# Kernel tuning notes

Hardware: AMD Instinct MI355X
Metric: run time of the kernel (lower is better)

## Reference

```python
import jax, jax.numpy as jnp
import numpy as np

B, L, D, H = 2, 256, 512, 8
DV = D // H
INF = 1e12

def _xavier(key, shape, fan_in, fan_out):
    a = float(np.sqrt(6.0 / (fan_in + fan_out)))
    return jax.random.uniform(key, shape, minval=-a, maxval=a, dtype=jnp.float32)

def setup_inputs() -> dict:
    key = jax.random.key(0)
    ks = jax.random.split(key, 9)
    inp = jax.random.normal(ks[0], (B, L, D), dtype=jnp.float32)
    relation_inp = jax.random.normal(ks[1], (B, L, L, D), dtype=jnp.float32)
    mask = jax.random.randint(ks[2], (B, L, L), 0, 2).astype(bool)
    adj_mask = jax.random.randint(ks[3], (B, H, L, L), 0, 2).astype(jnp.float32)
    W_value = _xavier(ks[4], (D, H * DV), D, H * DV)
    W_relation = _xavier(ks[5], (D, H * DV), D, H * DV)
    # weight vectors have torch shape (1,1,1,H,DV); xavier fans over last two dims
    w_src = _xavier(ks[6], (H, DV), H, DV)
    w_tgt = _xavier(ks[7], (H, DV), H, DV)
    w_rel = _xavier(ks[8], (H, DV), H, DV)
    return {"inp": inp, "relation_inp": relation_inp, "mask": mask,
            "adj_mask": adj_mask, "W_value": W_value, "W_relation": W_relation,
            "w_src": w_src, "w_tgt": w_tgt, "w_rel": w_rel}

def reference(inp, relation_inp, mask, adj_mask, W_value, W_relation, w_src, w_tgt, w_rel):
    b, l, d = inp.shape
    h, dv = w_src.shape
    # value: (B,H,L,DV)
    value = (inp @ W_value).reshape(b, l, h, dv).transpose(0, 2, 1, 3)
    # relation: (B,L,L,H,DV)
    relation = (relation_inp @ W_relation).reshape(b, l, l, h, dv)
    # scores[b,h,i,j] = w_src.v_j + w_tgt.v_i + w_rel.rel[b,i,j,h]
    s_src = jnp.einsum('bhjd,hd->bhj', value, w_src)[:, :, None, :]
    s_tgt = jnp.einsum('bhid,hd->bhi', value, w_tgt)[:, :, :, None]
    s_rel = jnp.einsum('bijhd,hd->bhij', relation, w_rel)
    scores = s_src + s_tgt + s_rel
    scores = jnp.where(scores >= 0, scores, 0.2 * scores)  # LeakyReLU(0.2)
    m = mask[:, None]  # (B,1,L,L)
    adj_zero = adj_mask == 0
    scores = jnp.where(m, -INF, scores)
    scores = jnp.where(adj_zero, -INF, scores)
    attn = jax.nn.softmax(scores, axis=-1)
    # normalized: divide by edge weight (zeros -> weight INF -> 1/INF)
    inv = jnp.where(adj_zero, 1.0 / INF, 1.0 / jnp.where(adj_zero, 1.0, adj_mask))
    attn = attn * inv
    attn = attn / jnp.maximum(jnp.sum(jnp.abs(attn), axis=-1, keepdims=True), 1e-12)
    attn = jnp.where(m, 0.0, attn)
    attn = jnp.where(adj_zero, 0.0, attn)
    out = jnp.einsum('bhij,bhjd->bhid', attn, value)
    out = out.transpose(0, 2, 1, 3).reshape(b, l, d)  # concat heads
    return out + inp
```

## Files before the change

kernel.cpp:

```cpp
#include <hip/hip_runtime.h>

#define B_ 2
#define L_ 256
#define D_ 512
#define H_ 8
#define DV_ 64
#define NEGINF 1e12f

#define WS_VALUE 0
#define WS_WR    262144
#define WS_SSRC  266240
#define WS_STGT  270336

#define GLOAD_LDS16(g, l)                                                     \
    __builtin_amdgcn_global_load_lds(                                         \
        (const __attribute__((address_space(1))) void*)(g),                   \
        (__attribute__((address_space(3))) void*)(l), 16, 0, 0)

__global__ __launch_bounds__(256) void k_wr(const float* __restrict__ Wrel,
                                            const float* __restrict__ wrel,
                                            float* __restrict__ WR) {
    int flat = blockIdx.x * 256 + threadIdx.x;
    int k = flat >> 3, h = flat & 7;
    const float* a = Wrel + k * 512 + h * 64;
    const float* b = wrel + h * 64;
    float s = 0.f;
#pragma unroll
    for (int d = 0; d < 64; d += 4) {
        float4 x = *(const float4*)(a + d);
        float4 y = *(const float4*)(b + d);
        s += x.x * y.x + x.y * y.y + x.z * y.z + x.w * y.w;
    }
    WR[k * 8 + h] = s;
}

__global__ __launch_bounds__(256) void k_value(const float* __restrict__ inp,
                                               const float* __restrict__ Wv,
                                               const float* __restrict__ wsrc,
                                               const float* __restrict__ wtgt,
                                               float* __restrict__ value,
                                               float* __restrict__ s_src,
                                               float* __restrict__ s_tgt) {
    int blk = blockIdx.x;
    int ct  = blk & 1;
    int rt  = blk >> 1;
    int n   = ct * 256 + threadIdx.x;
    int r0  = rt * 4;
    const float* i0 = inp + (size_t)(r0 + 0) * 512;
    const float* i1 = inp + (size_t)(r0 + 1) * 512;
    const float* i2 = inp + (size_t)(r0 + 2) * 512;
    const float* i3 = inp + (size_t)(r0 + 3) * 512;
    float a0 = 0.f, a1 = 0.f, a2 = 0.f, a3 = 0.f;
#pragma unroll 16
    for (int k = 0; k < 512; ++k) {
        float w = Wv[(size_t)k * 512 + n];
        a0 = fmaf(i0[k], w, a0);
        a1 = fmaf(i1[k], w, a1);
        a2 = fmaf(i2[k], w, a2);
        a3 = fmaf(i3[k], w, a3);
    }
    int h = n >> 6, dv = n & 63;
    float acc[4] = {a0, a1, a2, a3};
    float wsv = wsrc[h * 64 + dv];
    float wtv = wtgt[h * 64 + dv];
#pragma unroll
    for (int r = 0; r < 4; ++r) {
        int row = r0 + r;
        int b = row >> 8, l = row & 255;
        value[(((size_t)(b * 8 + h)) * 256 + l) * 64 + dv] = acc[r];
        float ss = acc[r] * wsv;
        float st = acc[r] * wtv;
#pragma unroll
        for (int off = 32; off >= 1; off >>= 1) {
            ss += __shfl_xor(ss, off);
            st += __shfl_xor(st, off);
        }
        if (dv == 0) {
            s_src[(size_t)(b * 8 + h) * 256 + l] = ss;
            s_tgt[(size_t)(b * 8 + h) * 256 + l] = st;
        }
    }
}

__global__ __launch_bounds__(256) void k_main(const float* __restrict__ rel,
                                              const int*   __restrict__ mask,
                                              const float* __restrict__ adj,
                                              const float* __restrict__ inp,
                                              const float* __restrict__ value,
                                              const float* __restrict__ WR,
                                              const float* __restrict__ s_src,
                                              const float* __restrict__ s_tgt,
                                              float* __restrict__ out) {
    __shared__ float lds[8192];
    int bi   = blockIdx.x;
    int b    = bi >> 8;
    int i    = bi & 255;
    int tid  = threadIdx.x;
    int w    = tid >> 6;
    int lane = tid & 63;

    const float* relbase = rel + (size_t)bi * 256 * 512;

    const float* gsrc[4];
    {
#pragma unroll
        for (int s = 0; s < 4; ++s) {
            int f = s * 64 + lane;
            int rl = f >> 2, c = f & 3;
            int r = w * 64 + rl;
            int cp = c ^ (r & 3);
            gsrc[s] = relbase + (size_t)r * 512 + cp * 4;
        }
    }

#define STAGE(bufofs, k0)                                                      \
    {                                                                          \
        _Pragma("unroll")                                                      \
        for (int s = 0; s < 4; ++s)                                            \
            GLOAD_LDS16(gsrc[s] + (k0), &lds[(bufofs) + w * 1024 + s * 256]);  \
    }

    float acc[8];
#pragma unroll
    for (int h = 0; h < 8; ++h) acc[h] = 0.f;

    int tswz = tid & 3;

    STAGE(0, 0);
    for (int kt = 0; kt < 32; ++kt) {
        int cur = (kt & 1) * 4096;
        if (kt < 31) {
            int nxt = ((kt + 1) & 1) * 4096;
            STAGE(nxt, (kt + 1) * 16);
            asm volatile("s_waitcnt vmcnt(4)" ::: "memory");
        } else {
            asm volatile("s_waitcnt vmcnt(0)" ::: "memory");
        }
        const float* myrow = &lds[cur + tid * 16];
        const float* wrt   = WR + kt * 16 * 8;
#pragma unroll
        for (int q = 0; q < 4; ++q) {
            float4 x = *(const float4*)&myrow[(q ^ tswz) << 2];
#pragma unroll
            for (int h = 0; h < 8; ++h) {
                acc[h] = fmaf(x.x, wrt[(q * 4 + 0) * 8 + h],
                         fmaf(x.y, wrt[(q * 4 + 1) * 8 + h],
                         fmaf(x.z, wrt[(q * 4 + 2) * 8 + h],
                         fmaf(x.w, wrt[(q * 4 + 3) * 8 + h], acc[h]))));
            }
        }
    }

    __syncthreads();
    float* srel_s = lds;
    float* attn_s = lds + 2048;
#pragma unroll
    for (int h = 0; h < 8; ++h) srel_s[h * 256 + tid] = acc[h];
    __syncthreads();

    {
        int h  = tid >> 5;
        int ln = tid & 31;
        float stgt = s_tgt[(size_t)(b * 8 + h) * 256 + i];
        const float* ssrc   = s_src + (size_t)(b * 8 + h) * 256;
        const float* adjrow = adj + ((size_t)(b * 8 + h) * 256 + i) * 256;
        const int*   mrow   = mask + (size_t)bi * 256;

        float sc[8], av[8];
        int mb = 0;
        float rowmax = -3.0e38f;
#pragma unroll
        for (int t = 0; t < 8; ++t) {
            int j = ln + 32 * t;
            float a = adjrow[j];
            av[t] = a;
            int m = mrow[j];
            float s = ssrc[j] + stgt + srel_s[h * 256 + j];
            s = (s >= 0.f) ? s : 0.2f * s;
            if (m != 0) { s = -NEGINF; mb |= (1 << t); }
            if (a == 0.f) s = -NEGINF;
            sc[t] = s;
            rowmax = fmaxf(rowmax, s);
        }
#pragma unroll
        for (int off = 16; off >= 1; off >>= 1)
            rowmax = fmaxf(rowmax, __shfl_xor(rowmax, off));

        float rowsum = 0.f;
#pragma unroll
        for (int t = 0; t < 8; ++t) {
            sc[t] = expf(sc[t] - rowmax);
            rowsum += sc[t];
        }
#pragma unroll
        for (int off = 16; off >= 1; off >>= 1)
            rowsum += __shfl_xor(rowsum, off);

        float sumabs = 0.f;
#pragma unroll
        for (int t = 0; t < 8; ++t) {
            float p = sc[t] / rowsum;
            float invv = (av[t] == 0.f) ? 1e-12f : (1.0f / av[t]);
            p *= invv;
            sc[t] = p;
            sumabs += fabsf(p);
        }
#pragma unroll
        for (int off = 16; off >= 1; off >>= 1)
            sumabs += __shfl_xor(sumabs, off);

        float rdn = 1.0f / fmaxf(sumabs, 1e-12f);
#pragma unroll
        for (int t = 0; t < 8; ++t) {
            float p = sc[t] * rdn;
            if (mb & (1 << t)) p = 0.f;
            if (av[t] == 0.f) p = 0.f;
            attn_s[h * 256 + ln + 32 * t] = p;
        }
    }
    __syncthreads();

    {
        int h  = tid >> 5;
        int d0 = (tid & 31) * 2;
        const float* vbase = value + ((size_t)(b * 8 + h) * 256) * 64 + d0;
        const float* arow  = attn_s + h * 256;
        float ax = 0.f, ay = 0.f;
#pragma unroll 8
        for (int j = 0; j < 256; ++j) {
            float a = arow[j];
            float2 v2 = *(const float2*)(vbase + (size_t)j * 64);
            ax = fmaf(a, v2.x, ax);
            ay = fmaf(a, v2.y, ay);
        }
        size_t o = (size_t)bi * 512 + h * 64 + d0;
        out[o]     = inp[o] + ax;
        out[o + 1] = inp[o + 1] + ay;
    }
}

extern "C" void kernel_launch(void* const* d_in, const int* in_sizes, int n_in,
                              void* d_out, int out_size, void* d_ws, size_t ws_size,
                              hipStream_t stream) {
    const float* inp      = (const float*)d_in[0];
    const float* rel      = (const float*)d_in[1];
    const int*   mask     = (const int*)  d_in[2];
    const float* adj      = (const float*)d_in[3];
    const float* W_value  = (const float*)d_in[4];
    const float* W_rel    = (const float*)d_in[5];
    const float* w_src    = (const float*)d_in[6];
    const float* w_tgt    = (const float*)d_in[7];
    const float* w_rel    = (const float*)d_in[8];
    float* out = (float*)d_out;

    float* ws    = (float*)d_ws;
    float* value = ws + WS_VALUE;
    float* WR    = ws + WS_WR;
    float* s_src = ws + WS_SSRC;
    float* s_tgt = ws + WS_STGT;

    k_wr<<<16, 256, 0, stream>>>(W_rel, w_rel, WR);
    k_value<<<256, 256, 0, stream>>>(inp, W_value, w_src, w_tgt,
                                     value, s_src, s_tgt);
    k_main<<<B_ * L_, 256, 0, stream>>>(rel, mask, adj, inp, value, WR,
                                        s_src, s_tgt, out);
}
```

Before: 118.4 us.

## Split relation-score reduction into a standalone register-resident streaming kernel

Moves the dominant reduction of the 512 MB relation tensor against the folded W_relation·w_rel weights out of the fused attention kernel into a separate kernel. Each wavefront streams 32 rows with direct float4 global loads and register-resident weights, reducing partial sums with cross-lane shuffles. The LDS double-buffered async-copy pipeline goes away, and the attention kernel reads precomputed scores from a workspace buffer. This adds an extra launch and a small global round trip for the scores, in exchange for better occupancy and memory-level parallelism on the bandwidth-bound stream. The softmax division is also replaced by one reciprocal followed by multiplies.

```diff
diff --git a/kernel.cpp b/kernel.cpp
--- a/kernel.cpp
+++ b/kernel.cpp
@@ -11,11 +11,7 @@
 #define WS_WR    262144
 #define WS_SSRC  266240
 #define WS_STGT  270336
-
-#define GLOAD_LDS16(g, l)                                                     \
-    __builtin_amdgcn_global_load_lds(                                         \
-        (const __attribute__((address_space(1))) void*)(g),                   \
-        (__attribute__((address_space(3))) void*)(l), 16, 0, 0)
+#define WS_SREL  274432
 
 __global__ __launch_bounds__(256) void k_wr(const float* __restrict__ Wrel,
                                             const float* __restrict__ wrel,
@@ -82,87 +78,100 @@
     }
 }
 
-__global__ __launch_bounds__(256) void k_main(const float* __restrict__ rel,
-                                              const int*   __restrict__ mask,
+__global__ __launch_bounds__(256, 3) void k_srel(const float* __restrict__ rel,
+                                                 const float* __restrict__ WR,
+                                                 float* __restrict__ srel) {
+    int tid  = threadIdx.x;
+    int lane = tid & 63;
+    int gw   = blockIdx.x * 4 + (tid >> 6);
+
+    float wa[32], wb[32];
+    {
+        const float4* wp = (const float4*)(WR + 32 * lane);
+        const float4* wq = (const float4*)(WR + 2048 + 32 * lane);
+#pragma unroll
+        for (int s = 0; s < 8; ++s) {
+            float4 t = wp[s];
+            wa[4 * s] = t.x; wa[4 * s + 1] = t.y; wa[4 * s + 2] = t.z; wa[4 * s + 3] = t.w;
+            float4 u = wq[s];
+            wb[4 * s] = u.x; wb[4 * s + 1] = u.y; wb[4 * s + 2] = u.z; wb[4 * s + 3] = u.w;
+        }
+    }
+
+    const float* rp = rel + (size_t)gw * 32 * 512 + lane * 4;
+
+#define LOADLO(j) (*(const float4*)(rp + (size_t)(j) * 512))
+#define LOADHI(j) (*(const float4*)(rp + (size_t)(j) * 512 + 256))
+
+#define ROW(lo, hi, jj)                                                        \
+    {                                                                          \
+        float A[8];                                                            \
+        _Pragma("unroll")                                                      \
+        for (int h = 0; h < 8; ++h) {                                          \
+            A[h] = fmaf(lo.x, wa[h],                                           \
+                   fmaf(lo.y, wa[8 + h],                                       \
+                   fmaf(lo.z, wa[16 + h],                                      \
+                   fmaf(lo.w, wa[24 + h],                                      \
+                   fmaf(hi.x, wb[h],                                           \
+                   fmaf(hi.y, wb[8 + h],                                       \
+                   fmaf(hi.z, wb[16 + h],                                      \
+                        hi.w * wb[24 + h])))))));                              \
+        }                                                                      \
+        _Pragma("unroll")                                                      \
+        for (int h = 0; h < 8; ++h) {                                          \
+            A[h] += __shfl_xor(A[h], 8);                                       \
+            A[h] += __shfl_xor(A[h], 16);                                      \
+            A[h] += __shfl_xor(A[h], 32);                                      \
+        }                                                                      \
+        int hi3 = lane >> 3;                                                   \
+        float v = A[0];                                                        \
+        _Pragma("unroll")                                                      \
+        for (int h = 1; h < 8; ++h) v = (hi3 == h) ? A[h] : v;                 \
+        v += __shfl_xor(v, 1);                                                 \
+        v += __shfl_xor(v, 2);                                                 \
+        v += __shfl_xor(v, 4);                                                 \
+        if ((lane & 7) == 0) {                                                 \
+            int R = gw * 32 + (jj);                                            \
+            srel[((size_t)(R >> 8)) * 2048 + hi3 * 256 + (R & 255)] = v;       \
+        }                                                                      \
+    }
+
+    float4 loA = LOADLO(0), hiA = LOADHI(0);
+    float4 loB = LOADLO(1), hiB = LOADHI(1);
+#pragma unroll 1
+    for (int jj = 0; jj < 32; jj += 2) {
+        float4 nloA, nhiA, nloB, nhiB;
+        if (jj + 2 < 32) { nloA = LOADLO(jj + 2); nhiA = LOADHI(jj + 2); }
+        if (jj + 3 < 32) { nloB = LOADLO(jj + 3); nhiB = LOADHI(jj + 3); }
+        ROW(loA, hiA, jj);
+        ROW(loB, hiB, jj + 1);
+        loA = nloA; hiA = nhiA; loB = nloB; hiB = nhiB;
+    }
+#undef ROW
+#undef LOADLO
+#undef LOADHI
+}
+
+__global__ __launch_bounds__(256) void k_attn(const int*   __restrict__ mask,
                                               const float* __restrict__ adj,
                                               const float* __restrict__ inp,
                                               const float* __restrict__ value,
-                                              const float* __restrict__ WR,
+                                              const float* __restrict__ srel,
                                               const float* __restrict__ s_src,
                                               const float* __restrict__ s_tgt,
                                               float* __restrict__ out) {
-    __shared__ float lds[8192];
-    int bi   = blockIdx.x;
-    int b    = bi >> 8;
-    int i    = bi & 255;
-    int tid  = threadIdx.x;
-    int w    = tid >> 6;
-    int lane = tid & 63;
-
-    const float* relbase = rel + (size_t)bi * 256 * 512;
-
-    const float* gsrc[4];
-    {
-#pragma unroll
-        for (int s = 0; s < 4; ++s) {
-            int f = s * 64 + lane;
-            int rl = f >> 2, c = f & 3;
-            int r = w * 64 + rl;
-            int cp = c ^ (r & 3);
-            gsrc[s] = relbase + (size_t)r * 512 + cp * 4;
-        }
-    }
-
-#define STAGE(bufofs, k0)                                                      \
-    {                                                                          \
-        _Pragma("unroll")                                                      \
-        for (int s = 0; s < 4; ++s)                                            \
-            GLOAD_LDS16(gsrc[s] + (k0), &lds[(bufofs) + w * 1024 + s * 256]);  \
-    }
-
-    float acc[8];
-#pragma unroll
-    for (int h = 0; h < 8; ++h) acc[h] = 0.f;
-
-    int tswz = tid & 3;
-
-    STAGE(0, 0);
-    for (int kt = 0; kt < 32; ++kt) {
-        int cur = (kt & 1) * 4096;
-        if (kt < 31) {
-            int nxt = ((kt + 1) & 1) * 4096;
-            STAGE(nxt, (kt + 1) * 16);
-            asm volatile("s_waitcnt vmcnt(4)" ::: "memory");
-        } else {
-            asm volatile("s_waitcnt vmcnt(0)" ::: "memory");
-        }
-        const float* myrow = &lds[cur + tid * 16];
-        const float* wrt   = WR + kt * 16 * 8;
-#pragma unroll
-        for (int q = 0; q < 4; ++q) {
-            float4 x = *(const float4*)&myrow[(q ^ tswz) << 2];
-#pragma unroll
-            for (int h = 0; h < 8; ++h) {
-                acc[h] = fmaf(x.x, wrt[(q * 4 + 0) * 8 + h],
-                         fmaf(x.y, wrt[(q * 4 + 1) * 8 + h],
-                         fmaf(x.z, wrt[(q * 4 + 2) * 8 + h],
-                         fmaf(x.w, wrt[(q * 4 + 3) * 8 + h], acc[h]))));
-            }
-        }
-    }
-
-    __syncthreads();
-    float* srel_s = lds;
-    float* attn_s = lds + 2048;
-#pragma unroll
-    for (int h = 0; h < 8; ++h) srel_s[h * 256 + tid] = acc[h];
-    __syncthreads();
+    __shared__ float attn_s[2048];
+    int bi  = blockIdx.x;
+    int b   = bi >> 8;
+    int i   = bi & 255;
+    int tid = threadIdx.x;
 
     {
         int h  = tid >> 5;
         int ln = tid & 31;
         float stgt = s_tgt[(size_t)(b * 8 + h) * 256 + i];
         const float* ssrc   = s_src + (size_t)(b * 8 + h) * 256;
+        const float* srl    = srel + (size_t)bi * 2048 + h * 256;
         const float* adjrow = adj + ((size_t)(b * 8 + h) * 256 + i) * 256;
         const int*   mrow   = mask + (size_t)bi * 256;
 
@@ -175,7 +184,7 @@
             float a = adjrow[j];
             av[t] = a;
             int m = mrow[j];
-            float s = ssrc[j] + stgt + srel_s[h * 256 + j];
+            float s = ssrc[j] + stgt + srl[j];
             s = (s >= 0.f) ? s : 0.2f * s;
             if (m != 0) { s = -NEGINF; mb |= (1 << t); }
             if (a == 0.f) s = -NEGINF;
@@ -195,11 +204,12 @@
 #pragma unroll
         for (int off = 16; off >= 1; off >>= 1)
             rowsum += __shfl_xor(rowsum, off);
+        float rinv = 1.0f / rowsum;
 
         float sumabs = 0.f;
 #pragma unroll
         for (int t = 0; t < 8; ++t) {
-            float p = sc[t] / rowsum;
+            float p = sc[t] * rinv;
             float invv = (av[t] == 0.f) ? 1e-12f : (1.0f / av[t]);
             p *= invv;
             sc[t] = p;
@@ -258,10 +268,12 @@
     float* WR    = ws + WS_WR;
     float* s_src = ws + WS_SSRC;
     float* s_tgt = ws + WS_STGT;
+    float* srel  = ws + WS_SREL;
 
     k_wr<<<16, 256, 0, stream>>>(W_rel, w_rel, WR);
+    k_srel<<<1024, 256, 0, stream>>>(rel, WR, srel);
     k_value<<<256, 256, 0, stream>>>(inp, W_value, w_src, w_tgt,
                                      value, s_src, s_tgt);
-    k_main<<<B_ * L_, 256, 0, stream>>>(rel, mask, adj, inp, value, WR,
+    k_attn<<<B_ * L_, 256, 0, stream>>>(mask, adj, inp, value, srel,
                                         s_src, s_tgt, out);
 }
```

Measured after the change: 125.0 us. 1.06x slower.

## Use dedicated producer wave with 4-deep LDS ring and flag sync

Applied to the files above, without the earlier changes.

Adds a fifth wavefront that only issues global-to-LDS loads of the relation tile into a 4-slot ring buffer. The four compute waves spin on per-stage ready flags and signal completion counters, replacing the lockstep double-buffered loop in which every wave both loaded and computed. The goal is deeper prefetch and overlap of the memory-bound relation stream with the FMA work. The cost is doubled LDS use (64KB), spin-wait overhead, and removal of the bank-conflict swizzle; the block now has 320 threads. It also replaces the division by rowsum with multiplication by its reciprocal.

```diff
diff --git a/kernel.cpp b/kernel.cpp
--- a/kernel.cpp
+++ b/kernel.cpp
@@ -82,83 +82,97 @@
     }
 }
 
-__global__ __launch_bounds__(256) void k_main(const float* __restrict__ rel,
-                                              const int*   __restrict__ mask,
-                                              const float* __restrict__ adj,
-                                              const float* __restrict__ inp,
-                                              const float* __restrict__ value,
-                                              const float* __restrict__ WR,
-                                              const float* __restrict__ s_src,
-                                              const float* __restrict__ s_tgt,
-                                              float* __restrict__ out) {
-    __shared__ float lds[8192];
+__global__ __launch_bounds__(320, 2) void k_main(const float* __restrict__ rel,
+                                                 const int*   __restrict__ mask,
+                                                 const float* __restrict__ adj,
+                                                 const float* __restrict__ inp,
+                                                 const float* __restrict__ value,
+                                                 const float* __restrict__ WR,
+                                                 const float* __restrict__ s_src,
+                                                 const float* __restrict__ s_tgt,
+                                                 float* __restrict__ out) {
+    __shared__ float ring[16384];
+    __shared__ int ready_s[32];
+    __shared__ int done_s[32];
     int bi   = blockIdx.x;
     int b    = bi >> 8;
     int i    = bi & 255;
     int tid  = threadIdx.x;
-    int w    = tid >> 6;
     int lane = tid & 63;
+    int wv   = tid >> 6;
 
     const float* relbase = rel + (size_t)bi * 256 * 512;
 
-    const float* gsrc[4];
-    {
-#pragma unroll
-        for (int s = 0; s < 4; ++s) {
-            int f = s * 64 + lane;
-            int rl = f >> 2, c = f & 3;
-            int r = w * 64 + rl;
-            int cp = c ^ (r & 3);
-            gsrc[s] = relbase + (size_t)r * 512 + cp * 4;
-        }
-    }
-
-#define STAGE(bufofs, k0)                                                      \
-    {                                                                          \
-        _Pragma("unroll")                                                      \
-        for (int s = 0; s < 4; ++s)                                            \
-            GLOAD_LDS16(gsrc[s] + (k0), &lds[(bufofs) + w * 1024 + s * 256]);  \
-    }
+    if (tid < 32) { ready_s[tid] = 0; done_s[tid] = 0; }
+    __syncthreads();
 
     float acc[8];
 #pragma unroll
     for (int h = 0; h < 8; ++h) acc[h] = 0.f;
 
-    int tswz = tid & 3;
-
-    STAGE(0, 0);
-    for (int kt = 0; kt < 32; ++kt) {
-        int cur = (kt & 1) * 4096;
-        if (kt < 31) {
-            int nxt = ((kt + 1) & 1) * 4096;
-            STAGE(nxt, (kt + 1) * 16);
-            asm volatile("s_waitcnt vmcnt(4)" ::: "memory");
-        } else {
-            asm volatile("s_waitcnt vmcnt(0)" ::: "memory");
-        }
-        const float* myrow = &lds[cur + tid * 16];
-        const float* wrt   = WR + kt * 16 * 8;
-#pragma unroll
-        for (int q = 0; q < 4; ++q) {
-            float4 x = *(const float4*)&myrow[(q ^ tswz) << 2];
-#pragma unroll
-            for (int h = 0; h < 8; ++h) {
-                acc[h] = fmaf(x.x, wrt[(q * 4 + 0) * 8 + h],
-                         fmaf(x.y, wrt[(q * 4 + 1) * 8 + h],
-                         fmaf(x.z, wrt[(q * 4 + 2) * 8 + h],
-                         fmaf(x.w, wrt[(q * 4 + 3) * 8 + h], acc[h]))));
+    if (wv == 4) {
+        const float* src0 = relbase + (size_t)(lane >> 2) * 512 + (lane & 3) * 4;
+        for (int t = 0; t < 32; ++t) {
+            if (t >= 4) {
+                while (__hip_atomic_load(&done_s[t - 4], __ATOMIC_ACQUIRE,
+                                         __HIP_MEMORY_SCOPE_WORKGROUP) < 4)
+                    __builtin_amdgcn_s_sleep(2);
             }
-        }
-    }
-
-    __syncthreads();
-    float* srel_s = lds;
-    float* attn_s = lds + 2048;
-#pragma unroll
-    for (int h = 0; h < 8; ++h) srel_s[h * 256 + tid] = acc[h];
-    __syncthreads();
-
-    {
+            const float* s = src0 + t * 16;
+            float* dst = &ring[(t & 3) * 4096];
+#pragma unroll
+            for (int ii = 0; ii < 16; ++ii)
+                GLOAD_LDS16(s + (size_t)ii * 16 * 512, dst + ii * 256);
+            if (t >= 2) {
+                asm volatile("s_waitcnt vmcnt(32)" ::: "memory");
+                if (lane == 0)
+                    __hip_atomic_store(&ready_s[t - 2], 1, __ATOMIC_RELEASE,
+                                       __HIP_MEMORY_SCOPE_WORKGROUP);
+            }
+        }
+        asm volatile("s_waitcnt vmcnt(16)" ::: "memory");
+        if (lane == 0)
+            __hip_atomic_store(&ready_s[30], 1, __ATOMIC_RELEASE,
+                               __HIP_MEMORY_SCOPE_WORKGROUP);
+        asm volatile("s_waitcnt vmcnt(0)" ::: "memory");
+        if (lane == 0)
+            __hip_atomic_store(&ready_s[31], 1, __ATOMIC_RELEASE,
+                               __HIP_MEMORY_SCOPE_WORKGROUP);
+    } else {
+        for (int t = 0; t < 32; ++t) {
+            while (__hip_atomic_load(&ready_s[t], __ATOMIC_ACQUIRE,
+                                     __HIP_MEMORY_SCOPE_WORKGROUP) == 0)
+                __builtin_amdgcn_s_sleep(2);
+            const float* myrow = &ring[(t & 3) * 4096 + tid * 16];
+            const float* wrt   = WR + t * 128;
+#pragma unroll
+            for (int q = 0; q < 4; ++q) {
+                float4 x = *(const float4*)(myrow + q * 4);
+#pragma unroll
+                for (int h = 0; h < 8; ++h) {
+                    acc[h] = fmaf(x.x, wrt[(q * 4 + 0) * 8 + h],
+                             fmaf(x.y, wrt[(q * 4 + 1) * 8 + h],
+                             fmaf(x.z, wrt[(q * 4 + 2) * 8 + h],
+                             fmaf(x.w, wrt[(q * 4 + 3) * 8 + h], acc[h]))));
+                }
+            }
+            asm volatile("s_waitcnt lgkmcnt(0)" ::: "memory");
+            if (lane == 0)
+                __hip_atomic_fetch_add(&done_s[t], 1, __ATOMIC_RELEASE,
+                                       __HIP_MEMORY_SCOPE_WORKGROUP);
+        }
+    }
+
+    __syncthreads();
+    float* srel_s = ring;
+    float* attn_s = ring + 2048;
+    if (tid < 256) {
+#pragma unroll
+        for (int h = 0; h < 8; ++h) srel_s[h * 256 + tid] = acc[h];
+    }
+    __syncthreads();
+
+    if (tid < 256) {
         int h  = tid >> 5;
         int ln = tid & 31;
         float stgt = s_tgt[(size_t)(b * 8 + h) * 256 + i];
@@ -195,11 +209,12 @@
 #pragma unroll
         for (int off = 16; off >= 1; off >>= 1)
             rowsum += __shfl_xor(rowsum, off);
+        float rinv = 1.0f / rowsum;
 
         float sumabs = 0.f;
 #pragma unroll
         for (int t = 0; t < 8; ++t) {
-            float p = sc[t] / rowsum;
+            float p = sc[t] * rinv;
             float invv = (av[t] == 0.f) ? 1e-12f : (1.0f / av[t]);
             p *= invv;
             sc[t] = p;
@@ -220,7 +235,7 @@
     }
     __syncthreads();
 
-    {
+    if (tid < 256) {
         int h  = tid >> 5;
         int d0 = (tid & 31) * 2;
         const float* vbase = value + ((size_t)(b * 8 + h) * 256) * 64 + d0;
@@ -262,6 +277,6 @@
     k_wr<<<16, 256, 0, stream>>>(W_rel, w_rel, WR);
     k_value<<<256, 256, 0, stream>>>(inp, W_value, w_src, w_tgt,
                                      value, s_src, s_tgt);
-    k_main<<<B_ * L_, 256, 0, stream>>>(rel, mask, adj, inp, value, WR,
+    k_main<<<B_ * L_, 320, 0, stream>>>(rel, mask, adj, inp, value, WR,
                                         s_src, s_tgt, out);
 }
```

Measured after the change: 138.6 us. 1.17x slower.
